# Kernel tuning notes

Measured on AMD Instinct MI355X. Metric: run time of the kernel, lower is better.

The kernel has to match this reference:

```python
import jax, jax.numpy as jnp
import numpy as np

B, I, O, P = 32, 2048, 64, 4  # batch, input caps, output caps, pose side
D = P * P
EPS = 1e-7
N_ITERS = 3

def setup_inputs() -> dict:
    key = jax.random.key(0)
    k1, k2, k3, k4, k5 = jax.random.split(key, 5)
    return {
        'input_poses': jax.random.normal(k1, (B, I, P, P), dtype=jnp.float32),
        'input_activations': jax.random.uniform(k2, (B, I), dtype=jnp.float32),
        'w': jax.random.normal(k3, (O, I, P, P), dtype=jnp.float32) * 0.05,
        'beta_a': jax.random.normal(k4, (1, O), dtype=jnp.float32),
        'beta_u': jax.random.normal(k5, (1, O), dtype=jnp.float32),
    }

def em_routing(V, a_in, beta_a, beta_u):
    # V: [B,O,I,D] votes, a_in: [B,I], beta_a/beta_u: [1,O]
    b, o, i, d = V.shape
    R = jnp.full((b, o, i), 1.0 / o, dtype=V.dtype)
    mu = None
    a_out = None
    for t in range(N_ITERS):
        inv_temp = 1.0 + t  # inverse temperature (lambda) schedule
        # ---- M-step ----
        r = R * a_in[:, None, :]                              # [B,O,I]
        r_sum = r.sum(axis=2, keepdims=True) + EPS            # [B,O,1]
        mu = jnp.einsum('boi,boid->bod', r, V) / r_sum        # [B,O,D]
        diff2 = (V - mu[:, :, None, :]) ** 2                  # [B,O,I,D]
        sigma2 = jnp.einsum('boi,boid->bod', r, diff2) / r_sum + EPS
        cost = (beta_u[:, :, None] + 0.5 * jnp.log(sigma2)) * r_sum  # [B,O,D]
        a_out = jax.nn.sigmoid(inv_temp * (beta_a - cost.sum(axis=-1)))  # [B,O]
        # ---- E-step ----
        if t < N_ITERS - 1:
            log_p = -0.5 * jnp.sum(diff2 / sigma2[:, :, None, :] + jnp.log(sigma2)[:, :, None, :], axis=-1)  # [B,O,I]
            R = jax.nn.softmax(jnp.log(a_out + EPS)[:, :, None] + log_p, axis=1)
    return mu, a_out

def reference(input_poses, input_activations, w, beta_a, beta_u):
    # votes: poses[B,1,I,P,P] @ w[O,I,P,P] -> [B,O,I,P,P]
    votes = jnp.einsum('bipq,oiqr->boipr', input_poses, w)
    V = votes.reshape(B, O, I, D)
    mu, a_out = em_routing(V, input_activations, beta_a, beta_u)
    capsule_poses = mu.reshape(B, O, P, P)
    return capsule_poses, a_out
```

## Files before the change

kernel.cpp:

```cpp
#include <hip/hip_runtime.h>
#include <stdint.h>

constexpr int Bn = 32, In = 2048;
constexpr float EPSF = 1e-7f;
constexpr int NC  = 32;
constexpr int IPB = In / NC;
constexpr int IPW = IPB / 4;

template <int CTRL>
__device__ __forceinline__ float dpp_add(float x) {
  int y = __builtin_amdgcn_update_dpp(0, __float_as_int(x), CTRL, 0xF, 0xF, true);
  return x + __int_as_float(y);
}

__device__ __forceinline__ float wave_sum64(float x) {
  x = dpp_add<0x121>(x);
  x = dpp_add<0x122>(x);
  x = dpp_add<0x124>(x);
  x = dpp_add<0x128>(x);
#if __has_builtin(__builtin_amdgcn_permlane16_swap)
  {
    auto pr = __builtin_amdgcn_permlane16_swap(__float_as_uint(x), __float_as_uint(x), false, false);
    x = __uint_as_float(pr[0]) + __uint_as_float(pr[1]);
  }
#else
  x += __int_as_float(__builtin_amdgcn_ds_swizzle(__float_as_int(x), 0x401F));
#endif
#if __has_builtin(__builtin_amdgcn_permlane32_swap)
  {
    auto pr = __builtin_amdgcn_permlane32_swap(__float_as_uint(x), __float_as_uint(x), false, false);
    x = __uint_as_float(pr[0]) + __uint_as_float(pr[1]);
  }
#else
  x += __shfl_xor(x, 32);
#endif
  return x;
}

__global__ __launch_bounds__(256) void transpose_w_k(const float4* __restrict__ w,
                                                     float4* __restrict__ w_t) {
  int idx = blockIdx.x * 256 + threadIdx.x;
  int o = idx >> 13;
  int rest = idx & 8191;
  int i = rest >> 2;
  int k = rest & 3;
  w_t[(size_t)((i << 2) + k) * 64 + o] = w[idx];
}

template <int TPASS>
__global__ __launch_bounds__(256)
__attribute__((amdgpu_waves_per_eu(4, 4)))
void pass_k(const float* __restrict__ poses,
            const float* __restrict__ a_in,
            const float* __restrict__ w_t,
            const float* __restrict__ params,
            float* __restrict__ partials) {
  const int gid = blockIdx.x;
  const int xcd = gid & 7;
  const int s   = gid >> 3;
  const int b   = s & 31;
  const int cc  = xcd * 4 + (s >> 5);
  const int tid = threadIdx.x, wv = tid >> 6, ln = tid & 63;
  const int i0 = __builtin_amdgcn_readfirstlane(cc * IPB + wv * IPW);

  float k0 = 0.f, k1[16], k2[16];
  if (TPASS > 0) {
    const float4* pp4 = (const float4*)(params + (size_t)(b * 64 + ln) * 36);
    float mu[16];
#pragma unroll
    for (int k = 0; k < 4; ++k) {
      float4 v = pp4[k];
      mu[4 * k] = v.x; mu[4 * k + 1] = v.y; mu[4 * k + 2] = v.z; mu[4 * k + 3] = v.w;
    }
#pragma unroll
    for (int k = 0; k < 4; ++k) {
      float4 v = pp4[4 + k];
      k2[4 * k] = v.x; k2[4 * k + 1] = v.y; k2[4 * k + 2] = v.z; k2[4 * k + 3] = v.w;
    }
    k0 = ((const float*)pp4)[32];
#pragma unroll
    for (int d = 0; d < 16; ++d) {
      k1[d] = 2.f * k2[d] * mu[d];
      k0 = fmaf(-k2[d], mu[d] * mu[d], k0);
    }
  }

  float rs = 0.f, S1[16], S2[16];
#pragma unroll
  for (int d = 0; d < 16; ++d) { S1[d] = 0.f; S2[d] = 0.f; }

  const float4* wt4 = (const float4*)w_t;
  const float* pbase = poses + ((size_t)b * In + i0) * 16;
  const float* abase = a_in + (size_t)b * In + i0;

  float4 cw0 = wt4[(size_t)(i0 * 4 + 0) * 64 + ln];
  float4 cw1 = wt4[(size_t)(i0 * 4 + 1) * 64 + ln];
  float4 cw2 = wt4[(size_t)(i0 * 4 + 2) * 64 + ln];
  float4 cw3 = wt4[(size_t)(i0 * 4 + 3) * 64 + ln];

#pragma unroll 4
  for (int ii = 0; ii < IPW; ++ii) {
    const int inx = (ii + 1 < IPW) ? (i0 + ii + 1) : (i0 + ii);
    float4 nw0 = wt4[(size_t)(inx * 4 + 0) * 64 + ln];
    float4 nw1 = wt4[(size_t)(inx * 4 + 1) * 64 + ln];
    float4 nw2 = wt4[(size_t)(inx * 4 + 2) * 64 + ln];
    float4 nw3 = wt4[(size_t)(inx * 4 + 3) * 64 + ln];

    const float4* pp = (const float4*)(pbase + ii * 16);
    float4 p0 = pp[0], p1 = pp[1], p2 = pp[2], p3 = pp[3];
    float V[16], q[16];
#define VROW(p, Pv)                                                                    \
    V[p * 4 + 0] = fmaf(Pv.w, cw3.x, fmaf(Pv.z, cw2.x, fmaf(Pv.y, cw1.x, Pv.x * cw0.x))); \
    V[p * 4 + 1] = fmaf(Pv.w, cw3.y, fmaf(Pv.z, cw2.y, fmaf(Pv.y, cw1.y, Pv.x * cw0.y))); \
    V[p * 4 + 2] = fmaf(Pv.w, cw3.z, fmaf(Pv.z, cw2.z, fmaf(Pv.y, cw1.z, Pv.x * cw0.z))); \
    V[p * 4 + 3] = fmaf(Pv.w, cw3.w, fmaf(Pv.z, cw2.w, fmaf(Pv.y, cw1.w, Pv.x * cw0.w)));
    VROW(0, p0) VROW(1, p1) VROW(2, p2) VROW(3, p3)
#undef VROW
#pragma unroll
    for (int d = 0; d < 16; ++d) q[d] = V[d] * V[d];

    const float a = abase[ii];
    float r;
    if (TPASS == 0) {
      r = a * 0.015625f;
    } else {
      float u0 = k0, u1 = 0.f, u2 = 0.f, u3 = 0.f;
#pragma unroll
      for (int j = 0; j < 4; ++j) {
        u0 = fmaf(-k2[j], q[j], fmaf(k1[j], V[j], u0));
        u1 = fmaf(-k2[4 + j], q[4 + j], fmaf(k1[4 + j], V[4 + j], u1));
        u2 = fmaf(-k2[8 + j], q[8 + j], fmaf(k1[8 + j], V[8 + j], u2));
        u3 = fmaf(-k2[12 + j], q[12 + j], fmaf(k1[12 + j], V[12 + j], u3));
      }
      float u = (u0 + u1) + (u2 + u3);
      float e = __expf(u);
      float ss = wave_sum64(e) + 1e-37f;
      r = a * e * __builtin_amdgcn_rcpf(ss);
    }
    rs += r;
#pragma unroll
    for (int d = 0; d < 16; ++d) {
      S1[d] = fmaf(r, V[d], S1[d]);
      S2[d] = fmaf(r, q[d], S2[d]);
    }
    cw0 = nw0; cw1 = nw1; cw2 = nw2; cw3 = nw3;
  }

  __shared__ float lds[4][33][64];
  lds[wv][0][ln] = rs;
#pragma unroll
  for (int d = 0; d < 16; ++d) {
    lds[wv][1 + d][ln] = S1[d];
    lds[wv][17 + d][ln] = S2[d];
  }
  __syncthreads();
  for (int idx = tid; idx < 33 * 64; idx += 256) {
    int j = idx >> 6, o = idx & 63;
    float ssum = lds[0][j][o] + lds[1][j][o] + lds[2][j][o] + lds[3][j][o];
    partials[((size_t)(b * NC + cc) * 33 + j) * 64 + o] = ssum;
  }
}

template <int TPASS>
__global__ __launch_bounds__(256) void fin_k(const float* __restrict__ partials,
                                             const float* __restrict__ beta_a,
                                             const float* __restrict__ beta_u,
                                             float* __restrict__ params,
                                             float* __restrict__ out) {
  const int b = blockIdx.x;
  const int tid = threadIdx.x;
  __shared__ float redL[33 * 64];
  for (int idx = tid; idx < 33 * 64; idx += 256) {
    const float* base = partials + (size_t)b * NC * 2112 + idx;
    float s = 0.f;
#pragma unroll 8
    for (int c = 0; c < NC; ++c) s += base[(size_t)c * 2112];
    redL[idx] = s;
  }
  __syncthreads();
  if (tid < 64) {
    const int o = tid;
    const float r_sum = redL[o] + EPSF;
    const float inv = 1.f / r_sum;
    float muv[16], sg[16], lsum = 0.f;
#pragma unroll
    for (int d = 0; d < 16; ++d) {
      float m = redL[(1 + d) * 64 + o] * inv;
      float s2 = fmaxf(redL[(17 + d) * 64 + o] * inv - m * m, 0.f) + EPSF;
      muv[d] = m; sg[d] = s2; lsum += logf(s2);
    }
    const float cost = (16.f * beta_u[o] + 0.5f * lsum) * r_sum;
    const float aout = 1.f / (1.f + __expf(-(float)(TPASS + 1) * (beta_a[o] - cost)));
    if (TPASS < 2) {
      float c0 = logf(aout + EPSF) - 0.5f * lsum;
      float mx = c0;
#pragma unroll
      for (int k = 1; k < 64; k <<= 1) mx = fmaxf(mx, __shfl_xor(mx, k));
      float* pp = params + (size_t)(b * 64 + o) * 36;
#pragma unroll
      for (int d = 0; d < 16; ++d) {
        pp[d] = muv[d];
        pp[16 + d] = 0.5f / sg[d];
      }
      pp[32] = c0 - mx;
    } else {
      const int g = b * 64 + o;
#pragma unroll
      for (int d = 0; d < 16; ++d) out[(size_t)g * 16 + d] = muv[d];
      out[Bn * 64 * 16 + g] = aout;
    }
  }
}

extern "C" void kernel_launch(void* const* d_in, const int* in_sizes, int n_in,
                              void* d_out, int out_size, void* d_ws, size_t ws_size,
                              hipStream_t stream) {
  const float* poses  = (const float*)d_in[0];
  const float* a_in   = (const float*)d_in[1];
  const float* w      = (const float*)d_in[2];
  const float* beta_a = (const float*)d_in[3];
  const float* beta_u = (const float*)d_in[4];
  float* out = (float*)d_out;

  float* w_t      = (float*)d_ws;
  float* partials = w_t + (size_t)In * 64 * 16;
  float* params   = partials + (size_t)Bn * NC * 33 * 64;

  transpose_w_k<<<dim3(In * 64 * 4 / 256), 256, 0, stream>>>((const float4*)w, (float4*)w_t);

  dim3 pg(Bn * NC);
  pass_k<0><<<pg, 256, 0, stream>>>(poses, a_in, w_t, params, partials);
  fin_k<0><<<Bn, 256, 0, stream>>>(partials, beta_a, beta_u, params, out);
  pass_k<1><<<pg, 256, 0, stream>>>(poses, a_in, w_t, params, partials);
  fin_k<1><<<Bn, 256, 0, stream>>>(partials, beta_a, beta_u, params, out);
  pass_k<2><<<pg, 256, 0, stream>>>(poses, a_in, w_t, params, partials);
  fin_k<2><<<Bn, 256, 0, stream>>>(partials, beta_a, beta_u, params, out);
}
```

Measured before the change: 194.1 us.

## Materialize votes once in bf16 and reuse across routing passes

Adds a votes kernel that computes the vote tensor once, stores it packed as bf16 in workspace and also does the first M-step. The later routing passes read these stored votes instead of recomputing them from poses and transformed weights. This trades the recomputation FMAs and weight loads for a large global write and two large global reads. It also adds bf16 rounding error to every vote, and changes the launch bounds.

```diff
diff --git a/kernel.cpp b/kernel.cpp
--- a/kernel.cpp
+++ b/kernel.cpp
@@ -37,6 +37,11 @@
   return x;
 }
 
+__device__ __forceinline__ uint32_t bfr(uint32_t u) { return u + 0x7fffu + ((u >> 16) & 1u); }
+__device__ __forceinline__ uint32_t packbf(float lo, float hi) {
+  return (bfr(__float_as_uint(lo)) >> 16) | (bfr(__float_as_uint(hi)) & 0xffff0000u);
+}
+
 __global__ __launch_bounds__(256) void transpose_w_k(const float4* __restrict__ w,
                                                      float4* __restrict__ w_t) {
   int idx = blockIdx.x * 256 + threadIdx.x;
@@ -47,14 +52,11 @@
   w_t[(size_t)((i << 2) + k) * 64 + o] = w[idx];
 }
 
-template <int TPASS>
-__global__ __launch_bounds__(256)
-__attribute__((amdgpu_waves_per_eu(4, 4)))
-void pass_k(const float* __restrict__ poses,
-            const float* __restrict__ a_in,
-            const float* __restrict__ w_t,
-            const float* __restrict__ params,
-            float* __restrict__ partials) {
+__global__ __launch_bounds__(256, 2) void votes_k(const float* __restrict__ poses,
+                                                  const float* __restrict__ a_in,
+                                                  const float* __restrict__ w_t,
+                                                  uint4* __restrict__ vb,
+                                                  float* __restrict__ partials) {
   const int gid = blockIdx.x;
   const int xcd = gid & 7;
   const int s   = gid >> 3;
@@ -63,8 +65,84 @@
   const int tid = threadIdx.x, wv = tid >> 6, ln = tid & 63;
   const int i0 = __builtin_amdgcn_readfirstlane(cc * IPB + wv * IPW);
 
-  float k0 = 0.f, k1[16], k2[16];
-  if (TPASS > 0) {
+  float rs = 0.f, S1[16], S2[16];
+#pragma unroll
+  for (int d = 0; d < 16; ++d) { S1[d] = 0.f; S2[d] = 0.f; }
+
+  const float4* wt4 = (const float4*)w_t;
+  const float* pbase = poses + ((size_t)b * In + i0) * 16;
+  const float* abase = a_in + (size_t)b * In + i0;
+  uint4* vbase = vb + (size_t)(b * In + i0) * 128 + ln;
+
+#pragma unroll 4
+  for (int ii = 0; ii < IPW; ++ii) {
+    const int i = i0 + ii;
+    float4 w0 = wt4[(size_t)(i * 4 + 0) * 64 + ln];
+    float4 w1 = wt4[(size_t)(i * 4 + 1) * 64 + ln];
+    float4 w2 = wt4[(size_t)(i * 4 + 2) * 64 + ln];
+    float4 w3 = wt4[(size_t)(i * 4 + 3) * 64 + ln];
+    const float4* pp = (const float4*)(pbase + ii * 16);
+    float4 p0 = pp[0], p1 = pp[1], p2 = pp[2], p3 = pp[3];
+    float V[16];
+#define VROW(p, Pv)                                                                  \
+    V[p * 4 + 0] = fmaf(Pv.w, w3.x, fmaf(Pv.z, w2.x, fmaf(Pv.y, w1.x, Pv.x * w0.x))); \
+    V[p * 4 + 1] = fmaf(Pv.w, w3.y, fmaf(Pv.z, w2.y, fmaf(Pv.y, w1.y, Pv.x * w0.y))); \
+    V[p * 4 + 2] = fmaf(Pv.w, w3.z, fmaf(Pv.z, w2.z, fmaf(Pv.y, w1.z, Pv.x * w0.z))); \
+    V[p * 4 + 3] = fmaf(Pv.w, w3.w, fmaf(Pv.z, w2.w, fmaf(Pv.y, w1.w, Pv.x * w0.w)));
+    VROW(0, p0) VROW(1, p1) VROW(2, p2) VROW(3, p3)
+#undef VROW
+    uint4 o0, o1;
+    o0.x = packbf(V[0], V[1]);  o0.y = packbf(V[2], V[3]);
+    o0.z = packbf(V[4], V[5]);  o0.w = packbf(V[6], V[7]);
+    o1.x = packbf(V[8], V[9]);  o1.y = packbf(V[10], V[11]);
+    o1.z = packbf(V[12], V[13]); o1.w = packbf(V[14], V[15]);
+    vbase[(size_t)ii * 128] = o0;
+    vbase[(size_t)ii * 128 + 64] = o1;
+    float Vr[16];
+    Vr[0] = __uint_as_float(o0.x << 16);  Vr[1] = __uint_as_float(o0.x & 0xffff0000u);
+    Vr[2] = __uint_as_float(o0.y << 16);  Vr[3] = __uint_as_float(o0.y & 0xffff0000u);
+    Vr[4] = __uint_as_float(o0.z << 16);  Vr[5] = __uint_as_float(o0.z & 0xffff0000u);
+    Vr[6] = __uint_as_float(o0.w << 16);  Vr[7] = __uint_as_float(o0.w & 0xffff0000u);
+    Vr[8] = __uint_as_float(o1.x << 16);  Vr[9] = __uint_as_float(o1.x & 0xffff0000u);
+    Vr[10] = __uint_as_float(o1.y << 16); Vr[11] = __uint_as_float(o1.y & 0xffff0000u);
+    Vr[12] = __uint_as_float(o1.z << 16); Vr[13] = __uint_as_float(o1.z & 0xffff0000u);
+    Vr[14] = __uint_as_float(o1.w << 16); Vr[15] = __uint_as_float(o1.w & 0xffff0000u);
+    const float r = abase[ii] * 0.015625f;
+    rs += r;
+#pragma unroll
+    for (int d = 0; d < 16; ++d) {
+      S1[d] = fmaf(r, Vr[d], S1[d]);
+      S2[d] = fmaf(r, Vr[d] * Vr[d], S2[d]);
+    }
+  }
+
+  __shared__ float lds[4][33][64];
+  lds[wv][0][ln] = rs;
+#pragma unroll
+  for (int d = 0; d < 16; ++d) {
+    lds[wv][1 + d][ln] = S1[d];
+    lds[wv][17 + d][ln] = S2[d];
+  }
+  __syncthreads();
+  for (int idx = tid; idx < 33 * 64; idx += 256) {
+    int j = idx >> 6, o = idx & 63;
+    float ssum = lds[0][j][o] + lds[1][j][o] + lds[2][j][o] + lds[3][j][o];
+    partials[((size_t)(b * NC + cc) * 33 + j) * 64 + o] = ssum;
+  }
+}
+
+__global__ __launch_bounds__(256, 2) void pass_k(const uint4* __restrict__ vb,
+                                                 const float* __restrict__ a_in,
+                                                 const float* __restrict__ params,
+                                                 float* __restrict__ partials) {
+  const int gid = blockIdx.x;
+  const int b = gid >> 5;
+  const int cc = gid & 31;
+  const int tid = threadIdx.x, wv = tid >> 6, ln = tid & 63;
+  const int i0 = __builtin_amdgcn_readfirstlane(cc * IPB + wv * IPW);
+
+  float k0, k1[16], k2[16];
+  {
     const float4* pp4 = (const float4*)(params + (size_t)(b * 64 + ln) * 36);
     float mu[16];
 #pragma unroll
@@ -89,61 +167,42 @@
 #pragma unroll
   for (int d = 0; d < 16; ++d) { S1[d] = 0.f; S2[d] = 0.f; }
 
-  const float4* wt4 = (const float4*)w_t;
-  const float* pbase = poses + ((size_t)b * In + i0) * 16;
   const float* abase = a_in + (size_t)b * In + i0;
-
-  float4 cw0 = wt4[(size_t)(i0 * 4 + 0) * 64 + ln];
-  float4 cw1 = wt4[(size_t)(i0 * 4 + 1) * 64 + ln];
-  float4 cw2 = wt4[(size_t)(i0 * 4 + 2) * 64 + ln];
-  float4 cw3 = wt4[(size_t)(i0 * 4 + 3) * 64 + ln];
+  const uint4* vbase = vb + (size_t)(b * In + i0) * 128 + ln;
 
 #pragma unroll 4
   for (int ii = 0; ii < IPW; ++ii) {
-    const int inx = (ii + 1 < IPW) ? (i0 + ii + 1) : (i0 + ii);
-    float4 nw0 = wt4[(size_t)(inx * 4 + 0) * 64 + ln];
-    float4 nw1 = wt4[(size_t)(inx * 4 + 1) * 64 + ln];
-    float4 nw2 = wt4[(size_t)(inx * 4 + 2) * 64 + ln];
-    float4 nw3 = wt4[(size_t)(inx * 4 + 3) * 64 + ln];
-
-    const float4* pp = (const float4*)(pbase + ii * 16);
-    float4 p0 = pp[0], p1 = pp[1], p2 = pp[2], p3 = pp[3];
+    uint4 a0 = vbase[(size_t)ii * 128];
+    uint4 a1 = vbase[(size_t)ii * 128 + 64];
     float V[16], q[16];
-#define VROW(p, Pv)                                                                    \
-    V[p * 4 + 0] = fmaf(Pv.w, cw3.x, fmaf(Pv.z, cw2.x, fmaf(Pv.y, cw1.x, Pv.x * cw0.x))); \
-    V[p * 4 + 1] = fmaf(Pv.w, cw3.y, fmaf(Pv.z, cw2.y, fmaf(Pv.y, cw1.y, Pv.x * cw0.y))); \
-    V[p * 4 + 2] = fmaf(Pv.w, cw3.z, fmaf(Pv.z, cw2.z, fmaf(Pv.y, cw1.z, Pv.x * cw0.z))); \
-    V[p * 4 + 3] = fmaf(Pv.w, cw3.w, fmaf(Pv.z, cw2.w, fmaf(Pv.y, cw1.w, Pv.x * cw0.w)));
-    VROW(0, p0) VROW(1, p1) VROW(2, p2) VROW(3, p3)
-#undef VROW
+    V[0] = __uint_as_float(a0.x << 16);  V[1] = __uint_as_float(a0.x & 0xffff0000u);
+    V[2] = __uint_as_float(a0.y << 16);  V[3] = __uint_as_float(a0.y & 0xffff0000u);
+    V[4] = __uint_as_float(a0.z << 16);  V[5] = __uint_as_float(a0.z & 0xffff0000u);
+    V[6] = __uint_as_float(a0.w << 16);  V[7] = __uint_as_float(a0.w & 0xffff0000u);
+    V[8] = __uint_as_float(a1.x << 16);  V[9] = __uint_as_float(a1.x & 0xffff0000u);
+    V[10] = __uint_as_float(a1.y << 16); V[11] = __uint_as_float(a1.y & 0xffff0000u);
+    V[12] = __uint_as_float(a1.z << 16); V[13] = __uint_as_float(a1.z & 0xffff0000u);
+    V[14] = __uint_as_float(a1.w << 16); V[15] = __uint_as_float(a1.w & 0xffff0000u);
 #pragma unroll
     for (int d = 0; d < 16; ++d) q[d] = V[d] * V[d];
-
-    const float a = abase[ii];
-    float r;
-    if (TPASS == 0) {
-      r = a * 0.015625f;
-    } else {
-      float u0 = k0, u1 = 0.f, u2 = 0.f, u3 = 0.f;
-#pragma unroll
-      for (int j = 0; j < 4; ++j) {
-        u0 = fmaf(-k2[j], q[j], fmaf(k1[j], V[j], u0));
-        u1 = fmaf(-k2[4 + j], q[4 + j], fmaf(k1[4 + j], V[4 + j], u1));
-        u2 = fmaf(-k2[8 + j], q[8 + j], fmaf(k1[8 + j], V[8 + j], u2));
-        u3 = fmaf(-k2[12 + j], q[12 + j], fmaf(k1[12 + j], V[12 + j], u3));
-      }
-      float u = (u0 + u1) + (u2 + u3);
-      float e = __expf(u);
-      float ss = wave_sum64(e) + 1e-37f;
-      r = a * e * __builtin_amdgcn_rcpf(ss);
-    }
+    float u0 = k0, u1 = 0.f, u2 = 0.f, u3 = 0.f;
+#pragma unroll
+    for (int j = 0; j < 4; ++j) {
+      u0 = fmaf(-k2[j], q[j], fmaf(k1[j], V[j], u0));
+      u1 = fmaf(-k2[4 + j], q[4 + j], fmaf(k1[4 + j], V[4 + j], u1));
+      u2 = fmaf(-k2[8 + j], q[8 + j], fmaf(k1[8 + j], V[8 + j], u2));
+      u3 = fmaf(-k2[12 + j], q[12 + j], fmaf(k1[12 + j], V[12 + j], u3));
+    }
+    float u = (u0 + u1) + (u2 + u3);
+    float e = __expf(u);
+    float ss = wave_sum64(e) + 1e-37f;
+    float r = abase[ii] * e * __builtin_amdgcn_rcpf(ss);
     rs += r;
 #pragma unroll
     for (int d = 0; d < 16; ++d) {
       S1[d] = fmaf(r, V[d], S1[d]);
       S2[d] = fmaf(r, q[d], S2[d]);
     }
-    cw0 = nw0; cw1 = nw1; cw2 = nw2; cw3 = nw3;
   }
 
   __shared__ float lds[4][33][64];
@@ -223,16 +282,17 @@
   float* out = (float*)d_out;
 
   float* w_t      = (float*)d_ws;
-  float* partials = w_t + (size_t)In * 64 * 16;
+  uint4* vb       = (uint4*)(w_t + (size_t)In * 64 * 16);
+  float* partials = (float*)(vb + (size_t)Bn * In * 128);
   float* params   = partials + (size_t)Bn * NC * 33 * 64;
 
   transpose_w_k<<<dim3(In * 64 * 4 / 256), 256, 0, stream>>>((const float4*)w, (float4*)w_t);
 
   dim3 pg(Bn * NC);
-  pass_k<0><<<pg, 256, 0, stream>>>(poses, a_in, w_t, params, partials);
+  votes_k<<<pg, 256, 0, stream>>>(poses, a_in, w_t, vb, partials);
   fin_k<0><<<Bn, 256, 0, stream>>>(partials, beta_a, beta_u, params, out);
-  pass_k<1><<<pg, 256, 0, stream>>>(poses, a_in, w_t, params, partials);
+  pass_k<<<pg, 256, 0, stream>>>(vb, a_in, params, partials);
   fin_k<1><<<Bn, 256, 0, stream>>>(partials, beta_a, beta_u, params, out);
-  pass_k<2><<<pg, 256, 0, stream>>>(poses, a_in, w_t, params, partials);
+  pass_k<<<pg, 256, 0, stream>>>(vb, a_in, params, partials);
   fin_k<2><<<Bn, 256, 0, stream>>>(partials, beta_a, beta_u, params, out);
 }
```

New measurement: 197.4 us. About the same (+1.7%).

## Split routing pass into responsibility kernel and accumulation kernel with materialized R

Applied to the files above, without the earlier changes.

Splits each fused routing pass into two kernels. The first computes and stores the normalized responsibilities to a global buffer of size B*I*O. The second recomputes the votes and accumulates the weighted sums, combining the four waves with LDS atomics instead of a staged reduction. It also doubles the number of input chunks, drops the weight prefetch double buffering and relaxes the occupancy hint, aiming to lower register pressure per kernel. In exchange it recomputes the votes twice per iteration, adds 16 MB of R writes and reads plus extra launches, and doubles the partials that fin_k must reduce.

```diff
diff --git a/kernel.cpp b/kernel.cpp
--- a/kernel.cpp
+++ b/kernel.cpp
@@ -3,7 +3,7 @@
 
 constexpr int Bn = 32, In = 2048;
 constexpr float EPSF = 1e-7f;
-constexpr int NC  = 32;
+constexpr int NC  = 64;
 constexpr int IPB = In / NC;
 constexpr int IPW = IPB / 4;
 
@@ -47,24 +47,34 @@
   w_t[(size_t)((i << 2) + k) * 64 + o] = w[idx];
 }
 
-template <int TPASS>
+#define DECODE_BLOCK()                                   \
+  const int gid = blockIdx.x;                            \
+  const int xcd = gid & 7;                               \
+  const int s   = gid >> 3;                              \
+  const int b   = s & 31;                                \
+  const int cc  = xcd * 8 + (s >> 5);                    \
+  const int tid = threadIdx.x, wv = tid >> 6, ln = tid & 63; \
+  const int i0 = __builtin_amdgcn_readfirstlane(cc * IPB + wv * IPW);
+
+#define LOADW(i)                                         \
+  float4 w0 = wt4[(size_t)((i) * 4 + 0) * 64 + ln];      \
+  float4 w1 = wt4[(size_t)((i) * 4 + 1) * 64 + ln];      \
+  float4 w2 = wt4[(size_t)((i) * 4 + 2) * 64 + ln];      \
+  float4 w3 = wt4[(size_t)((i) * 4 + 3) * 64 + ln];
+#define VROW(p, Pv)                                                                  \
+  V[p * 4 + 0] = fmaf(Pv.w, w3.x, fmaf(Pv.z, w2.x, fmaf(Pv.y, w1.x, Pv.x * w0.x))); \
+  V[p * 4 + 1] = fmaf(Pv.w, w3.y, fmaf(Pv.z, w2.y, fmaf(Pv.y, w1.y, Pv.x * w0.y))); \
+  V[p * 4 + 2] = fmaf(Pv.w, w3.z, fmaf(Pv.z, w2.z, fmaf(Pv.y, w1.z, Pv.x * w0.z))); \
+  V[p * 4 + 3] = fmaf(Pv.w, w3.w, fmaf(Pv.z, w2.w, fmaf(Pv.y, w1.w, Pv.x * w0.w)));
+
 __global__ __launch_bounds__(256)
-__attribute__((amdgpu_waves_per_eu(4, 4)))
-void pass_k(const float* __restrict__ poses,
-            const float* __restrict__ a_in,
-            const float* __restrict__ w_t,
-            const float* __restrict__ params,
-            float* __restrict__ partials) {
-  const int gid = blockIdx.x;
-  const int xcd = gid & 7;
-  const int s   = gid >> 3;
-  const int b   = s & 31;
-  const int cc  = xcd * 4 + (s >> 5);
-  const int tid = threadIdx.x, wv = tid >> 6, ln = tid & 63;
-  const int i0 = __builtin_amdgcn_readfirstlane(cc * IPB + wv * IPW);
-
-  float k0 = 0.f, k1[16], k2[16];
-  if (TPASS > 0) {
+__attribute__((amdgpu_waves_per_eu(5)))
+void pass_a(const float* __restrict__ poses, const float* __restrict__ a_in,
+            const float* __restrict__ w_t, const float* __restrict__ params,
+            float* __restrict__ rbuf) {
+  DECODE_BLOCK()
+  float k0, k1[16], k2[16];
+  {
     const float4* pp4 = (const float4*)(params + (size_t)(b * 64 + ln) * 36);
     float mu[16];
 #pragma unroll
@@ -84,81 +94,81 @@
       k0 = fmaf(-k2[d], mu[d] * mu[d], k0);
     }
   }
-
-  float rs = 0.f, S1[16], S2[16];
-#pragma unroll
-  for (int d = 0; d < 16; ++d) { S1[d] = 0.f; S2[d] = 0.f; }
-
   const float4* wt4 = (const float4*)w_t;
   const float* pbase = poses + ((size_t)b * In + i0) * 16;
   const float* abase = a_in + (size_t)b * In + i0;
-
-  float4 cw0 = wt4[(size_t)(i0 * 4 + 0) * 64 + ln];
-  float4 cw1 = wt4[(size_t)(i0 * 4 + 1) * 64 + ln];
-  float4 cw2 = wt4[(size_t)(i0 * 4 + 2) * 64 + ln];
-  float4 cw3 = wt4[(size_t)(i0 * 4 + 3) * 64 + ln];
+  float* rbase = rbuf + ((size_t)b * In + i0) * 64 + ln;
 
 #pragma unroll 4
   for (int ii = 0; ii < IPW; ++ii) {
-    const int inx = (ii + 1 < IPW) ? (i0 + ii + 1) : (i0 + ii);
-    float4 nw0 = wt4[(size_t)(inx * 4 + 0) * 64 + ln];
-    float4 nw1 = wt4[(size_t)(inx * 4 + 1) * 64 + ln];
-    float4 nw2 = wt4[(size_t)(inx * 4 + 2) * 64 + ln];
-    float4 nw3 = wt4[(size_t)(inx * 4 + 3) * 64 + ln];
-
+    const int i = i0 + ii;
+    LOADW(i)
     const float4* pp = (const float4*)(pbase + ii * 16);
     float4 p0 = pp[0], p1 = pp[1], p2 = pp[2], p3 = pp[3];
-    float V[16], q[16];
-#define VROW(p, Pv)                                                                    \
-    V[p * 4 + 0] = fmaf(Pv.w, cw3.x, fmaf(Pv.z, cw2.x, fmaf(Pv.y, cw1.x, Pv.x * cw0.x))); \
-    V[p * 4 + 1] = fmaf(Pv.w, cw3.y, fmaf(Pv.z, cw2.y, fmaf(Pv.y, cw1.y, Pv.x * cw0.y))); \
-    V[p * 4 + 2] = fmaf(Pv.w, cw3.z, fmaf(Pv.z, cw2.z, fmaf(Pv.y, cw1.z, Pv.x * cw0.z))); \
-    V[p * 4 + 3] = fmaf(Pv.w, cw3.w, fmaf(Pv.z, cw2.w, fmaf(Pv.y, cw1.w, Pv.x * cw0.w)));
+    float V[16];
     VROW(0, p0) VROW(1, p1) VROW(2, p2) VROW(3, p3)
-#undef VROW
-#pragma unroll
-    for (int d = 0; d < 16; ++d) q[d] = V[d] * V[d];
-
-    const float a = abase[ii];
-    float r;
-    if (TPASS == 0) {
-      r = a * 0.015625f;
-    } else {
-      float u0 = k0, u1 = 0.f, u2 = 0.f, u3 = 0.f;
-#pragma unroll
-      for (int j = 0; j < 4; ++j) {
-        u0 = fmaf(-k2[j], q[j], fmaf(k1[j], V[j], u0));
-        u1 = fmaf(-k2[4 + j], q[4 + j], fmaf(k1[4 + j], V[4 + j], u1));
-        u2 = fmaf(-k2[8 + j], q[8 + j], fmaf(k1[8 + j], V[8 + j], u2));
-        u3 = fmaf(-k2[12 + j], q[12 + j], fmaf(k1[12 + j], V[12 + j], u3));
-      }
-      float u = (u0 + u1) + (u2 + u3);
-      float e = __expf(u);
-      float ss = wave_sum64(e) + 1e-37f;
-      r = a * e * __builtin_amdgcn_rcpf(ss);
-    }
+    float u0 = k0, u1 = 0.f, u2 = 0.f, u3 = 0.f;
+#pragma unroll
+    for (int j = 0; j < 4; ++j) {
+      u0 = fmaf(-k2[j], V[j] * V[j], fmaf(k1[j], V[j], u0));
+      u1 = fmaf(-k2[4 + j], V[4 + j] * V[4 + j], fmaf(k1[4 + j], V[4 + j], u1));
+      u2 = fmaf(-k2[8 + j], V[8 + j] * V[8 + j], fmaf(k1[8 + j], V[8 + j], u2));
+      u3 = fmaf(-k2[12 + j], V[12 + j] * V[12 + j], fmaf(k1[12 + j], V[12 + j], u3));
+    }
+    float u = (u0 + u1) + (u2 + u3);
+    float e = __expf(u);
+    float ss = wave_sum64(e) + 1e-37f;
+    rbase[(size_t)ii * 64] = abase[ii] * e * __builtin_amdgcn_rcpf(ss);
+  }
+}
+
+template <bool FIRST>
+__global__ __launch_bounds__(256)
+__attribute__((amdgpu_waves_per_eu(5)))
+void pass_b(const float* __restrict__ poses, const float* __restrict__ a_in,
+            const float* __restrict__ w_t, const float* __restrict__ rbuf,
+            float* __restrict__ partials) {
+  DECODE_BLOCK()
+  float rs = 0.f, S1[16], S2[16];
+#pragma unroll
+  for (int d = 0; d < 16; ++d) { S1[d] = 0.f; S2[d] = 0.f; }
+
+  const float4* wt4 = (const float4*)w_t;
+  const float* pbase = poses + ((size_t)b * In + i0) * 16;
+  const float* abase = a_in + (size_t)b * In + i0;
+  const float* rbase = rbuf + ((size_t)b * In + i0) * 64 + ln;
+
+  __shared__ float acc[33 * 64];
+  for (int j = tid; j < 33 * 64; j += 256) acc[j] = 0.f;
+
+#pragma unroll 4
+  for (int ii = 0; ii < IPW; ++ii) {
+    const int i = i0 + ii;
+    LOADW(i)
+    const float4* pp = (const float4*)(pbase + ii * 16);
+    float4 p0 = pp[0], p1 = pp[1], p2 = pp[2], p3 = pp[3];
+    float V[16];
+    VROW(0, p0) VROW(1, p1) VROW(2, p2) VROW(3, p3)
+    const float r = FIRST ? (abase[ii] * 0.015625f) : rbase[(size_t)ii * 64];
     rs += r;
 #pragma unroll
     for (int d = 0; d < 16; ++d) {
-      S1[d] = fmaf(r, V[d], S1[d]);
-      S2[d] = fmaf(r, q[d], S2[d]);
-    }
-    cw0 = nw0; cw1 = nw1; cw2 = nw2; cw3 = nw3;
-  }
-
-  __shared__ float lds[4][33][64];
-  lds[wv][0][ln] = rs;
+      float t1 = r * V[d];
+      S1[d] += t1;
+      S2[d] = fmaf(t1, V[d], S2[d]);
+    }
+  }
+
+  __syncthreads();
+  atomicAdd(&acc[ln], rs);
 #pragma unroll
   for (int d = 0; d < 16; ++d) {
-    lds[wv][1 + d][ln] = S1[d];
-    lds[wv][17 + d][ln] = S2[d];
+    atomicAdd(&acc[(1 + d) * 64 + ln], S1[d]);
+    atomicAdd(&acc[(17 + d) * 64 + ln], S2[d]);
   }
   __syncthreads();
-  for (int idx = tid; idx < 33 * 64; idx += 256) {
-    int j = idx >> 6, o = idx & 63;
-    float ssum = lds[0][j][o] + lds[1][j][o] + lds[2][j][o] + lds[3][j][o];
-    partials[((size_t)(b * NC + cc) * 33 + j) * 64 + o] = ssum;
-  }
+  for (int j = tid; j < 33 * 64; j += 256)
+    partials[(size_t)(b * NC + cc) * 2112 + j] = acc[j];
 }
 
 template <int TPASS>
@@ -223,16 +233,19 @@
   float* out = (float*)d_out;
 
   float* w_t      = (float*)d_ws;
-  float* partials = w_t + (size_t)In * 64 * 16;
+  float* rbuf     = w_t + (size_t)In * 64 * 16;
+  float* partials = rbuf + (size_t)Bn * In * 64;
   float* params   = partials + (size_t)Bn * NC * 33 * 64;
 
   transpose_w_k<<<dim3(In * 64 * 4 / 256), 256, 0, stream>>>((const float4*)w, (float4*)w_t);
 
   dim3 pg(Bn * NC);
-  pass_k<0><<<pg, 256, 0, stream>>>(poses, a_in, w_t, params, partials);
+  pass_b<true><<<pg, 256, 0, stream>>>(poses, a_in, w_t, rbuf, partials);
   fin_k<0><<<Bn, 256, 0, stream>>>(partials, beta_a, beta_u, params, out);
-  pass_k<1><<<pg, 256, 0, stream>>>(poses, a_in, w_t, params, partials);
+  pass_a<<<pg, 256, 0, stream>>>(poses, a_in, w_t, params, rbuf);
+  pass_b<false><<<pg, 256, 0, stream>>>(poses, a_in, w_t, rbuf, partials);
   fin_k<1><<<Bn, 256, 0, stream>>>(partials, beta_a, beta_u, params, out);
-  pass_k<2><<<pg, 256, 0, stream>>>(poses, a_in, w_t, params, partials);
+  pass_a<<<pg, 256, 0, stream>>>(poses, a_in, w_t, params, rbuf);
+  pass_b<false><<<pg, 256, 0, stream>>>(poses, a_in, w_t, rbuf, partials);
   fin_k<2><<<Bn, 256, 0, stream>>>(partials, beta_a, beta_u, params, out);
 }
```

Measured after the change: 497.1 us. 2.56x slower.
